# Kernel optimization log

Hardware: AMD Instinct MI355X
Metric: run time of the kernel (lower is better)

The kernel has to match this reference:

```python
import jax, jax.numpy as jnp
import numpy as np

N_NODES = 50000
EPS = 1e-5


def gcn_conv(x, src, dst, ew, W, b):
    # PyG GCNConv (self-loops already appended by caller):
    # deg computed at target, symmetric normalization, linear, scatter-add.
    deg = jax.ops.segment_sum(ew, dst, num_segments=N_NODES)          # [N]
    dinv = jnp.where(deg > 0, jax.lax.rsqrt(jnp.maximum(deg, 1e-12)), 0.0)
    norm = dinv[src] * ew * dinv[dst]                                 # [E]
    h = x @ W                                                         # [N, F_out]
    msg = norm[:, None] * h[src]                                      # [E, F_out] gather
    out = jax.ops.segment_sum(msg, dst, num_segments=N_NODES)        # scatter-add
    return out + b


def layer_norm(x, gamma, beta):
    mu = jnp.mean(x, axis=-1, keepdims=True)
    var = jnp.mean(jnp.square(x - mu), axis=-1, keepdims=True)
    return (x - mu) * jax.lax.rsqrt(var + EPS) * gamma + beta


def setup_inputs() -> dict:
    key = jax.random.key(0)
    ks = jax.random.split(key, 8)
    N, E, D, H = N_NODES, 800000, 128, 256
    x = jax.random.normal(ks[0], (N, D), dtype=jnp.float32)
    edge_index = jax.random.randint(ks[1], (2, E), 0, N, dtype=jnp.int32)
    edge_weight = jax.random.uniform(ks[2], (E,), dtype=jnp.float32)
    # Glorot-ish init for weights, zeros for biases.
    W1 = jax.random.normal(ks[3], (D, H), dtype=jnp.float32) / np.sqrt(D)
    b1 = jnp.zeros((H,), dtype=jnp.float32)
    W2 = jax.random.normal(ks[4], (H, D), dtype=jnp.float32) / np.sqrt(H)
    b2 = jnp.zeros((D,), dtype=jnp.float32)
    gamma = jnp.ones((D,), dtype=jnp.float32)
    beta = jnp.zeros((D,), dtype=jnp.float32)
    return {"x": x, "edge_index": edge_index, "edge_weight": edge_weight,
            "W1": W1, "b1": b1, "W2": W2, "b2": b2,
            "gamma": gamma, "beta": beta}


def reference(x, edge_index, edge_weight, W1, b1, W2, b2, gamma, beta):
    N = x.shape[0]
    # Add self-loops with weight 1 (PyG default), shared by both layers.
    loops = jnp.arange(N, dtype=edge_index.dtype)
    src = jnp.concatenate([edge_index[0], loops])
    dst = jnp.concatenate([edge_index[1], loops])
    ew = jnp.concatenate([edge_weight, jnp.ones((N,), dtype=edge_weight.dtype)])

    h = gcn_conv(x, src, dst, ew, W1, b1)      # [N, hidden]
    h = jax.nn.relu(h)
    h = gcn_conv(h, src, dst, ew, W2, b2)      # [N, input_dim]
    return layer_norm(h, gamma, beta)
```

## Files before the change

kernel.cpp:

```cpp
#include <hip/hip_runtime.h>


#define TPB 256
#define SLOT 64

typedef __bf16 bf16;
typedef __bf16 bf16x2 __attribute__((ext_vector_type(2)));
typedef __bf16 bf16x4 __attribute__((ext_vector_type(4)));
typedef __bf16 bf16x8 __attribute__((ext_vector_type(8)));
typedef float  f32x4  __attribute__((ext_vector_type(4)));

__global__ void k_fill_prep(const int* __restrict__ dst, const int* __restrict__ src,
                            const float* __restrict__ ew,
                            unsigned long long* deg64,
                            unsigned int* __restrict__ csr, int E,
                            const float* __restrict__ x, bf16* __restrict__ x_bf,
                            const float* __restrict__ W1, bf16* __restrict__ W1T,
                            const float* __restrict__ W2, bf16* __restrict__ W2T,
                            int n4, int nw, int D, int H) {
  int i = blockIdx.x * TPB + threadIdx.x;
  if (i < E) {
    int d = dst[i];
    float wf = ew[i];
    unsigned long long add =
        ((unsigned long long)1 << 32) |
        (unsigned long long)(unsigned int)(wf * 65536.0f + 0.5f);
    unsigned long long old = atomicAdd(&deg64[d], add);
    unsigned int pos = (unsigned int)(old >> 32);
    if (pos < SLOT) {
      unsigned int wb = __float_as_uint((float)(bf16)wf) & 0xFFFF0000u;
      csr[((size_t)d << 6) | pos] = wb | (unsigned int)src[i];
    }
  }
  if (i < nw) {
    int r1 = i / H, c1 = i % H;
    W1T[(size_t)c1 * D + r1] = (bf16)W1[i];
    int r2 = i / D, c2 = i % D;
    W2T[(size_t)c2 * H + r2] = (bf16)W2[i];
  }
  if (i < n4) {
    float4 v = reinterpret_cast<const float4*>(x)[i];
    bf16x4 o;
    o.x = (bf16)v.x; o.y = (bf16)v.y; o.z = (bf16)v.z; o.w = (bf16)v.w;
    reinterpret_cast<bf16x4*>(x_bf)[i] = o;
  }
}

__global__ void k_deg(const unsigned long long* __restrict__ deg64,
                      float* __restrict__ dinv, int* __restrict__ cnt, int N) {
  int i = blockIdx.x * TPB + threadIdx.x;
  if (i < N) {
    unsigned long long v = deg64[i];
    unsigned int c = (unsigned int)(v >> 32);
    float d = 1.0f + (float)(v & 0xFFFFFFFFull) * (1.0f / 65536.0f);
    dinv[i] = rsqrtf(d);
    cnt[i] = (c < SLOT) ? (int)c : SLOT;
  }
}

__global__ __launch_bounds__(256) void k_gemm_mfma(
    const bf16* __restrict__ A, const bf16* __restrict__ BT,
    const float* __restrict__ bias, int relu, int M, int K, int NC,
    bf16* __restrict__ Cb) {
  const int l = threadIdx.x & 63, w = threadIdx.x >> 6;
  const int c = l & 15, g = l >> 4;
  const int m0 = blockIdx.x * 64 + w * 16;
  const int n0 = blockIdx.y * 128;

  int ra = m0 + c;  if (ra >= M) ra = M - 1;
  const bf16* pa  = A + (size_t)ra * K + g * 8;
  const bf16* pb0 = BT + (size_t)(n0 + c) * K + g * 8;

  f32x4 acc[8] = {};
  for (int k0 = 0; k0 < K; k0 += 32) {
    bf16x8 a = *reinterpret_cast<const bf16x8*>(pa + k0);
#pragma unroll
    for (int nb = 0; nb < 8; ++nb) {
      bf16x8 b = *reinterpret_cast<const bf16x8*>(pb0 + (size_t)(nb * 16) * K + k0);
      acc[nb] = __builtin_amdgcn_mfma_f32_16x16x32_bf16(b, a, acc[nb], 0, 0, 0);
    }
  }

  int row = m0 + c;
  if (row < M) {
#pragma unroll
    for (int ni = 0; ni < 8; ++ni) {
      int col0 = n0 + ni * 16 + g * 4;
      f32x4 v = acc[ni];
      float4 bv = make_float4(0.f, 0.f, 0.f, 0.f);
      if (bias) bv = *reinterpret_cast<const float4*>(bias + col0);
      float o0 = v[0] + bv.x, o1 = v[1] + bv.y;
      float o2 = v[2] + bv.z, o3 = v[3] + bv.w;
      if (relu) {
        o0 = fmaxf(o0, 0.f); o1 = fmaxf(o1, 0.f);
        o2 = fmaxf(o2, 0.f); o3 = fmaxf(o3, 0.f);
      }
      bf16x4 ob;
      ob.x = (bf16)o0; ob.y = (bf16)o1; ob.z = (bf16)o2; ob.w = (bf16)o3;
      *reinterpret_cast<bf16x4*>(Cb + (size_t)row * NC + col0) = ob;
    }
  }
}

#define UNPACK_EDGE(e, w, v)                                                   \
  float w = __uint_as_float((e) & 0xFFFF0000u) * dinv[(e) & 0xFFFFu];          \
  bf16x2 v = *reinterpret_cast<const bf16x2*>(h + (size_t)((e) & 0xFFFFu) * F + c2);

__global__ __launch_bounds__(256) void k_agg_x(
    const bf16* __restrict__ h, const float* __restrict__ dinv,
    const int* __restrict__ cnt, const unsigned int* __restrict__ csr,
    bf16* __restrict__ out, int N) {
  const int F = 128;
  int wid = threadIdx.x >> 6, lane = threadIdx.x & 63;
  int node = blockIdx.x * 4 + wid;
  if (node >= N) return;
  float di = dinv[node];
  int c2 = lane << 1;
  bf16x2 hv = *reinterpret_cast<const bf16x2*>(h + (size_t)node * F + c2);
  float nx = 0.f, ny = 0.f;
  const unsigned int* cp = csr + ((size_t)node << 6);
  int n = cnt[node];
  int j = 0;
  for (; j + 8 <= n; j += 8) {
    uint4 q0 = *reinterpret_cast<const uint4*>(cp + j);
    uint4 q1 = *reinterpret_cast<const uint4*>(cp + j + 4);
    UNPACK_EDGE(q0.x, w0, v0) UNPACK_EDGE(q0.y, w1, v1)
    UNPACK_EDGE(q0.z, w2, v2) UNPACK_EDGE(q0.w, w3, v3)
    UNPACK_EDGE(q1.x, w4, v4) UNPACK_EDGE(q1.y, w5, v5)
    UNPACK_EDGE(q1.z, w6, v6) UNPACK_EDGE(q1.w, w7, v7)
    nx += w0 * (float)v0.x + w1 * (float)v1.x + w2 * (float)v2.x + w3 * (float)v3.x
        + w4 * (float)v4.x + w5 * (float)v5.x + w6 * (float)v6.x + w7 * (float)v7.x;
    ny += w0 * (float)v0.y + w1 * (float)v1.y + w2 * (float)v2.y + w3 * (float)v3.y
        + w4 * (float)v4.y + w5 * (float)v5.y + w6 * (float)v6.y + w7 * (float)v7.y;
  }
  for (; j < n; ++j) {
    unsigned int e = cp[j];
    UNPACK_EDGE(e, w, v)
    nx += w * (float)v.x; ny += w * (float)v.y;
  }
  float sw = di * di;
  float ax = sw * (float)hv.x + di * nx;
  float ay = sw * (float)hv.y + di * ny;
  bf16x2 o; o.x = (bf16)ax; o.y = (bf16)ay;
  *reinterpret_cast<bf16x2*>(out + (size_t)node * F + c2) = o;
}

__global__ __launch_bounds__(256) void k_agg2_ln(
    const bf16* __restrict__ h, const float* __restrict__ dinv,
    const int* __restrict__ cnt, const unsigned int* __restrict__ csr,
    const float* __restrict__ b2, const float* __restrict__ gamma,
    const float* __restrict__ beta, float* __restrict__ out, int N) {
  const int F = 128;
  int wid = threadIdx.x >> 6, lane = threadIdx.x & 63;
  int node = blockIdx.x * 4 + wid;
  if (node >= N) return;
  float di = dinv[node];
  int c2 = lane << 1;
  float2 bb = *reinterpret_cast<const float2*>(b2 + c2);
  bf16x2 hv = *reinterpret_cast<const bf16x2*>(h + (size_t)node * F + c2);
  float nx = 0.f, ny = 0.f;
  const unsigned int* cp = csr + ((size_t)node << 6);
  int n = cnt[node];
  int j = 0;
  for (; j + 8 <= n; j += 8) {
    uint4 q0 = *reinterpret_cast<const uint4*>(cp + j);
    uint4 q1 = *reinterpret_cast<const uint4*>(cp + j + 4);
    UNPACK_EDGE(q0.x, w0, v0) UNPACK_EDGE(q0.y, w1, v1)
    UNPACK_EDGE(q0.z, w2, v2) UNPACK_EDGE(q0.w, w3, v3)
    UNPACK_EDGE(q1.x, w4, v4) UNPACK_EDGE(q1.y, w5, v5)
    UNPACK_EDGE(q1.z, w6, v6) UNPACK_EDGE(q1.w, w7, v7)
    nx += w0 * (float)v0.x + w1 * (float)v1.x + w2 * (float)v2.x + w3 * (float)v3.x
        + w4 * (float)v4.x + w5 * (float)v5.x + w6 * (float)v6.x + w7 * (float)v7.x;
    ny += w0 * (float)v0.y + w1 * (float)v1.y + w2 * (float)v2.y + w3 * (float)v3.y
        + w4 * (float)v4.y + w5 * (float)v5.y + w6 * (float)v6.y + w7 * (float)v7.y;
  }
  for (; j < n; ++j) {
    unsigned int e = cp[j];
    UNPACK_EDGE(e, w, v)
    nx += w * (float)v.x; ny += w * (float)v.y;
  }
  float sw = di * di;
  float ax = bb.x + sw * (float)hv.x + di * nx;
  float ay = bb.y + sw * (float)hv.y + di * ny;
  float s  = ax + ay;
  float ss = ax * ax + ay * ay;
  for (int m = 32; m > 0; m >>= 1) {
    s  += __shfl_xor(s, m, 64);
    ss += __shfl_xor(ss, m, 64);
  }
  float mu  = s * (1.0f / 128.0f);
  float var = ss * (1.0f / 128.0f) - mu * mu;
  float inv = rsqrtf(var + 1e-5f);
  float2 g  = *reinterpret_cast<const float2*>(gamma + c2);
  float2 be = *reinterpret_cast<const float2*>(beta + c2);
  float2 o;
  o.x = (ax - mu) * inv * g.x + be.x;
  o.y = (ay - mu) * inv * g.y + be.y;
  *reinterpret_cast<float2*>(out + (size_t)node * F + c2) = o;
}

extern "C" void kernel_launch(void* const* d_in, const int* in_sizes, int n_in,
                              void* d_out, int out_size, void* d_ws, size_t ws_size,
                              hipStream_t stream) {
  const float* x     = (const float*)d_in[0];
  const int*   ei    = (const int*)d_in[1];
  const float* ew    = (const float*)d_in[2];
  const float* W1    = (const float*)d_in[3];
  const float* b1    = (const float*)d_in[4];
  const float* W2    = (const float*)d_in[5];
  const float* b2    = (const float*)d_in[6];
  const float* gamma = (const float*)d_in[7];
  const float* beta  = (const float*)d_in[8];
  float* out = (float*)d_out;

  const int D = 128, H = 256;
  const int N = in_sizes[0] / D;
  const int E = in_sizes[2];
  const int* src = ei;
  const int* dst = ei + E;

  char* p = (char*)d_ws;
  auto carve = [&](size_t bytes) -> void* {
    void* r = (void*)p;
    p += (bytes + 255) & ~(size_t)255;
    return r;
  };
  float*              dinv  = (float*)carve((size_t)N * 4);
  int*                cnt   = (int*)  carve((size_t)N * 4);
  unsigned long long* deg64 = (unsigned long long*)carve((size_t)N * 8);
  unsigned int*       csr   = (unsigned int*)carve((size_t)N * SLOT * 4);
  bf16*               x_bf  = (bf16*) carve((size_t)N * D * 2);
  bf16*               axb   = (bf16*) carve((size_t)N * D * 2);
  bf16*               out1  = (bf16*) carve((size_t)N * H * 2);
  bf16*               h2    = (bf16*) carve((size_t)N * D * 2);
  bf16*               W1T   = (bf16*) carve((size_t)D * H * 2);
  bf16*               W2T   = (bf16*) carve((size_t)H * D * 2);

  const int gN = (N + TPB - 1) / TPB;
  const int n4 = N * D / 4;
  const int nw = D * H;
  const int gE = (E + TPB - 1) / TPB;
  const int gP = (n4 + TPB - 1) / TPB;
  const int gF = (gE > gP) ? gE : gP;

  hipMemsetAsync(deg64, 0, (size_t)N * 8, stream);
  k_fill_prep<<<gF, TPB, 0, stream>>>(dst, src, ew, deg64, csr, E,
                                      x, x_bf, W1, W1T, W2, W2T, n4, nw, D, H);
  k_deg<<<gN, TPB, 0, stream>>>(deg64, dinv, cnt, N);

  k_agg_x<<<(N + 3) / 4, TPB, 0, stream>>>(x_bf, dinv, cnt, csr, axb, N);
  dim3 g1((N + 63) / 64, H / 128);
  k_gemm_mfma<<<g1, TPB, 0, stream>>>(axb, W1T, b1, 1, N, D, H, out1);

  dim3 g2((N + 63) / 64, D / 128);
  k_gemm_mfma<<<g2, TPB, 0, stream>>>(out1, W2T, nullptr, 0, N, H, D, h2);
  k_agg2_ln<<<(N + 3) / 4, TPB, 0, stream>>>(h2, dinv, cnt, csr,
                                             b2, gamma, beta, out, N);
}
```

Before: 213.0 us.

## Fuse first aggregation and both GEMMs into one kernel via shared memory

Replaces the separate aggregation kernel and the two MFMA GEMM launches with one kernel. Each block aggregates 16 nodes into LDS, runs the W1 GEMM with bias and ReLU into LDS, then runs the W2 GEMM and writes h2. This removes the global round-trips for the aggregated features and the N×256 hidden activation, plus two launches. In exchange, each 16-row block re-reads W1T and W2T from global/L2, the GEMM tiles are small, and each wave now processes four nodes in sequence during aggregation, which may lower latency hiding.

```diff
diff --git a/kernel.cpp b/kernel.cpp
--- a/kernel.cpp
+++ b/kernel.cpp
@@ -58,91 +58,107 @@
   }
 }
 
-__global__ __launch_bounds__(256) void k_gemm_mfma(
-    const bf16* __restrict__ A, const bf16* __restrict__ BT,
-    const float* __restrict__ bias, int relu, int M, int K, int NC,
-    bf16* __restrict__ Cb) {
-  const int l = threadIdx.x & 63, w = threadIdx.x >> 6;
-  const int c = l & 15, g = l >> 4;
-  const int m0 = blockIdx.x * 64 + w * 16;
-  const int n0 = blockIdx.y * 128;
-
-  int ra = m0 + c;  if (ra >= M) ra = M - 1;
-  const bf16* pa  = A + (size_t)ra * K + g * 8;
-  const bf16* pb0 = BT + (size_t)(n0 + c) * K + g * 8;
-
-  f32x4 acc[8] = {};
-  for (int k0 = 0; k0 < K; k0 += 32) {
-    bf16x8 a = *reinterpret_cast<const bf16x8*>(pa + k0);
-#pragma unroll
-    for (int nb = 0; nb < 8; ++nb) {
-      bf16x8 b = *reinterpret_cast<const bf16x8*>(pb0 + (size_t)(nb * 16) * K + k0);
-      acc[nb] = __builtin_amdgcn_mfma_f32_16x16x32_bf16(b, a, acc[nb], 0, 0, 0);
-    }
-  }
-
-  int row = m0 + c;
-  if (row < M) {
-#pragma unroll
-    for (int ni = 0; ni < 8; ++ni) {
-      int col0 = n0 + ni * 16 + g * 4;
-      f32x4 v = acc[ni];
-      float4 bv = make_float4(0.f, 0.f, 0.f, 0.f);
-      if (bias) bv = *reinterpret_cast<const float4*>(bias + col0);
-      float o0 = v[0] + bv.x, o1 = v[1] + bv.y;
-      float o2 = v[2] + bv.z, o3 = v[3] + bv.w;
-      if (relu) {
-        o0 = fmaxf(o0, 0.f); o1 = fmaxf(o1, 0.f);
-        o2 = fmaxf(o2, 0.f); o3 = fmaxf(o3, 0.f);
-      }
-      bf16x4 ob;
-      ob.x = (bf16)o0; ob.y = (bf16)o1; ob.z = (bf16)o2; ob.w = (bf16)o3;
-      *reinterpret_cast<bf16x4*>(Cb + (size_t)row * NC + col0) = ob;
-    }
-  }
-}
-
 #define UNPACK_EDGE(e, w, v)                                                   \
   float w = __uint_as_float((e) & 0xFFFF0000u) * dinv[(e) & 0xFFFFu];          \
   bf16x2 v = *reinterpret_cast<const bf16x2*>(h + (size_t)((e) & 0xFFFFu) * F + c2);
 
-__global__ __launch_bounds__(256) void k_agg_x(
-    const bf16* __restrict__ h, const float* __restrict__ dinv,
+__global__ __launch_bounds__(256) void k_agg_gemm(
+    const bf16* __restrict__ h , const float* __restrict__ dinv,
     const int* __restrict__ cnt, const unsigned int* __restrict__ csr,
-    bf16* __restrict__ out, int N) {
-  const int F = 128;
-  int wid = threadIdx.x >> 6, lane = threadIdx.x & 63;
-  int node = blockIdx.x * 4 + wid;
-  if (node >= N) return;
-  float di = dinv[node];
-  int c2 = lane << 1;
-  bf16x2 hv = *reinterpret_cast<const bf16x2*>(h + (size_t)node * F + c2);
-  float nx = 0.f, ny = 0.f;
-  const unsigned int* cp = csr + ((size_t)node << 6);
-  int n = cnt[node];
-  int j = 0;
-  for (; j + 8 <= n; j += 8) {
-    uint4 q0 = *reinterpret_cast<const uint4*>(cp + j);
-    uint4 q1 = *reinterpret_cast<const uint4*>(cp + j + 4);
-    UNPACK_EDGE(q0.x, w0, v0) UNPACK_EDGE(q0.y, w1, v1)
-    UNPACK_EDGE(q0.z, w2, v2) UNPACK_EDGE(q0.w, w3, v3)
-    UNPACK_EDGE(q1.x, w4, v4) UNPACK_EDGE(q1.y, w5, v5)
-    UNPACK_EDGE(q1.z, w6, v6) UNPACK_EDGE(q1.w, w7, v7)
-    nx += w0 * (float)v0.x + w1 * (float)v1.x + w2 * (float)v2.x + w3 * (float)v3.x
-        + w4 * (float)v4.x + w5 * (float)v5.x + w6 * (float)v6.x + w7 * (float)v7.x;
-    ny += w0 * (float)v0.y + w1 * (float)v1.y + w2 * (float)v2.y + w3 * (float)v3.y
-        + w4 * (float)v4.y + w5 * (float)v5.y + w6 * (float)v6.y + w7 * (float)v7.y;
-  }
-  for (; j < n; ++j) {
-    unsigned int e = cp[j];
-    UNPACK_EDGE(e, w, v)
-    nx += w * (float)v.x; ny += w * (float)v.y;
-  }
-  float sw = di * di;
-  float ax = sw * (float)hv.x + di * nx;
-  float ay = sw * (float)hv.y + di * ny;
-  bf16x2 o; o.x = (bf16)ax; o.y = (bf16)ay;
-  *reinterpret_cast<bf16x2*>(out + (size_t)node * F + c2) = o;
+    const bf16* __restrict__ W1T, const float* __restrict__ b1,
+    const bf16* __restrict__ W2T, bf16* __restrict__ h2, int N) {
+  const int F = 128, H = 256;
+  __shared__ bf16 axs[16][136];
+  __shared__ bf16 o1s[16][264];
+  const int wid = threadIdx.x >> 6, lane = threadIdx.x & 63;
+  const int c = lane & 15, g = lane >> 4;
+  const int c2 = lane << 1;
+
+  for (int t = 0; t < 4; ++t) {
+    int r = wid * 4 + t;
+    int node = blockIdx.x * 16 + r;
+    float ax = 0.f, ay = 0.f;
+    if (node < N) {
+      float di = dinv[node];
+      bf16x2 hv = *reinterpret_cast<const bf16x2*>(h + (size_t)node * F + c2);
+      float nx = 0.f, ny = 0.f;
+      const unsigned int* cp = csr + ((size_t)node << 6);
+      int n = cnt[node];
+      int j = 0;
+      for (; j + 8 <= n; j += 8) {
+        uint4 q0 = *reinterpret_cast<const uint4*>(cp + j);
+        uint4 q1 = *reinterpret_cast<const uint4*>(cp + j + 4);
+        UNPACK_EDGE(q0.x, w0, v0) UNPACK_EDGE(q0.y, w1, v1)
+        UNPACK_EDGE(q0.z, w2, v2) UNPACK_EDGE(q0.w, w3, v3)
+        UNPACK_EDGE(q1.x, w4, v4) UNPACK_EDGE(q1.y, w5, v5)
+        UNPACK_EDGE(q1.z, w6, v6) UNPACK_EDGE(q1.w, w7, v7)
+        nx += w0 * (float)v0.x + w1 * (float)v1.x + w2 * (float)v2.x + w3 * (float)v3.x
+            + w4 * (float)v4.x + w5 * (float)v5.x + w6 * (float)v6.x + w7 * (float)v7.x;
+        ny += w0 * (float)v0.y + w1 * (float)v1.y + w2 * (float)v2.y + w3 * (float)v3.y
+            + w4 * (float)v4.y + w5 * (float)v5.y + w6 * (float)v6.y + w7 * (float)v7.y;
+      }
+      for (; j < n; ++j) {
+        unsigned int e = cp[j];
+        UNPACK_EDGE(e, w, v)
+        nx += w * (float)v.x; ny += w * (float)v.y;
+      }
+      float sw = di * di;
+      ax = sw * (float)hv.x + di * nx;
+      ay = sw * (float)hv.y + di * ny;
+    }
+    bf16x2 o; o.x = (bf16)ax; o.y = (bf16)ay;
+    *reinterpret_cast<bf16x2*>(&axs[r][c2]) = o;
+  }
+  __syncthreads();
+
+  {
+    f32x4 acc[4] = {};
+    for (int k0 = 0; k0 < 128; k0 += 32) {
+      bf16x8 a = *reinterpret_cast<const bf16x8*>(&axs[c][k0 + g * 8]);
+#pragma unroll
+      for (int ni = 0; ni < 4; ++ni) {
+        int ncol = wid * 64 + ni * 16 + c;
+        bf16x8 b = *reinterpret_cast<const bf16x8*>(W1T + (size_t)ncol * F + k0 + g * 8);
+        acc[ni] = __builtin_amdgcn_mfma_f32_16x16x32_bf16(b, a, acc[ni], 0, 0, 0);
+      }
+    }
+#pragma unroll
+    for (int ni = 0; ni < 4; ++ni) {
+      int col0 = wid * 64 + ni * 16 + g * 4;
+      float4 bv = *reinterpret_cast<const float4*>(b1 + col0);
+      f32x4 v = acc[ni];
+      float o0 = fmaxf(v[0] + bv.x, 0.f), o1 = fmaxf(v[1] + bv.y, 0.f);
+      float o2 = fmaxf(v[2] + bv.z, 0.f), o3 = fmaxf(v[3] + bv.w, 0.f);
+      bf16x4 ob;
+      ob.x = (bf16)o0; ob.y = (bf16)o1; ob.z = (bf16)o2; ob.w = (bf16)o3;
+      *reinterpret_cast<bf16x4*>(&o1s[c][col0]) = ob;
+    }
+  }
+  __syncthreads();
+
+  {
+    f32x4 acc[2] = {};
+    for (int k0 = 0; k0 < 256; k0 += 32) {
+      bf16x8 a = *reinterpret_cast<const bf16x8*>(&o1s[c][k0 + g * 8]);
+#pragma unroll
+      for (int ni = 0; ni < 2; ++ni) {
+        int ncol = wid * 32 + ni * 16 + c;
+        bf16x8 b = *reinterpret_cast<const bf16x8*>(W2T + (size_t)ncol * H + k0 + g * 8);
+        acc[ni] = __builtin_amdgcn_mfma_f32_16x16x32_bf16(b, a, acc[ni], 0, 0, 0);
+      }
+    }
+    int node = blockIdx.x * 16 + c;
+    if (node < N) {
+#pragma unroll
+      for (int ni = 0; ni < 2; ++ni) {
+        int col0 = wid * 32 + ni * 16 + g * 4;
+        f32x4 v = acc[ni];
+        bf16x4 ob;
+        ob.x = (bf16)v[0]; ob.y = (bf16)v[1]; ob.z = (bf16)v[2]; ob.w = (bf16)v[3];
+        *reinterpret_cast<bf16x4*>(h2 + (size_t)node * F + col0) = ob;
+      }
+    }
+  }
 }
 
 __global__ __launch_bounds__(256) void k_agg2_ln(
@@ -230,8 +246,6 @@
   unsigned long long* deg64 = (unsigned long long*)carve((size_t)N * 8);
   unsigned int*       csr   = (unsigned int*)carve((size_t)N * SLOT * 4);
   bf16*               x_bf  = (bf16*) carve((size_t)N * D * 2);
-  bf16*               axb   = (bf16*) carve((size_t)N * D * 2);
-  bf16*               out1  = (bf16*) carve((size_t)N * H * 2);
   bf16*               h2    = (bf16*) carve((size_t)N * D * 2);
   bf16*               W1T   = (bf16*) carve((size_t)D * H * 2);
   bf16*               W2T   = (bf16*) carve((size_t)H * D * 2);
@@ -248,12 +262,9 @@
                                       x, x_bf, W1, W1T, W2, W2T, n4, nw, D, H);
   k_deg<<<gN, TPB, 0, stream>>>(deg64, dinv, cnt, N);
 
-  k_agg_x<<<(N + 3) / 4, TPB, 0, stream>>>(x_bf, dinv, cnt, csr, axb, N);
-  dim3 g1((N + 63) / 64, H / 128);
-  k_gemm_mfma<<<g1, TPB, 0, stream>>>(axb, W1T, b1, 1, N, D, H, out1);
-
-  dim3 g2((N + 63) / 64, D / 128);
-  k_gemm_mfma<<<g2, TPB, 0, stream>>>(out1, W2T, nullptr, 0, N, H, D, h2);
+  k_agg_gemm<<<(N + 15) / 16, TPB, 0, stream>>>(x_bf, dinv, cnt, csr,
+                                                W1T, b1, W2T, h2, N);
+
   k_agg2_ln<<<(N + 3) / 4, TPB, 0, stream>>>(h2, dinv, cnt, csr,
                                              b2, gamma, beta, out, N);
 }
```

After: 193.8 us. 1.1x faster.
